# Kernel tuning notes

Hardware: AMD Instinct MI355X
Metric: run time of the kernel (lower is better)

The kernel has to match this reference:

```python
import math
import jax, jax.numpy as jnp
import numpy as np

N_NODES = 50000
N_EDGES = 600000
D = 128          # in_dim == out_dim
T = 4            # num_types
R = 4            # num_relations
H = 8            # n_heads
DK = D // H
MAX_LEN = 240    # RelTemporalEncoding max_len
EPS = 1e-5


def _sinusoid_table(n_hid, max_len):
    pos = jnp.arange(max_len, dtype=jnp.float32)[:, None]
    div = jnp.exp(jnp.arange(0, n_hid, 2, dtype=jnp.float32) * (-math.log(10000.0) / n_hid))
    s = jnp.sin(pos * div) / math.sqrt(n_hid)
    c = jnp.cos(pos * div) / math.sqrt(n_hid)
    emb = jnp.zeros((max_len, n_hid), dtype=jnp.float32)
    emb = emb.at[:, 0::2].set(s).at[:, 1::2].set(c)
    return emb


def setup_inputs() -> dict:
    key = jax.random.key(0)
    ks = jax.random.split(key, 24)
    f32 = jnp.float32
    inp = {
        'node_inp': jax.random.normal(ks[0], (N_NODES, D), dtype=f32),
        'node_type': jax.random.randint(ks[1], (N_NODES,), 0, T),
        'edge_index': jax.random.randint(ks[2], (2, N_EDGES), 0, N_NODES),
        'edge_type': jax.random.randint(ks[3], (N_EDGES,), 0, R),
        'edge_time': jax.random.randint(ks[4], (N_EDGES,), 0, MAX_LEN),
        # per-type Linear weights stored as [T, in, out] (x @ W + b)
        'Wk': jax.random.normal(ks[5], (T, D, D), dtype=f32) * 0.05,
        'bk': jnp.zeros((T, D), dtype=f32),
        'Wq': jax.random.normal(ks[6], (T, D, D), dtype=f32) * 0.05,
        'bq': jnp.zeros((T, D), dtype=f32),
        'Wv': jax.random.normal(ks[7], (T, D, D), dtype=f32) * 0.05,
        'bv': jnp.zeros((T, D), dtype=f32),
        'Wa': jax.random.normal(ks[8], (T, D, D), dtype=f32) * 0.05,
        'ba': jnp.zeros((T, D), dtype=f32),
        'gamma': jnp.ones((T, D), dtype=f32),
        'beta': jnp.zeros((T, D), dtype=f32),
        'rel_pri': jnp.ones((R, H), dtype=f32),
        'rel_att': jax.random.normal(ks[9], (R, H, DK, DK), dtype=f32) * 0.1,
        'rel_msg': jax.random.normal(ks[10], (R, H, DK, DK), dtype=f32) * 0.1,
        'skip': jnp.ones((T,), dtype=f32),
        'rte_W': jax.random.normal(ks[11], (D, D), dtype=f32) * 0.05,
        'rte_b': jnp.zeros((D,), dtype=f32),
    }
    return inp


def _type_proj(x, W, b, types):
    # all-type projection [T, N, D] then gather per-node type (T is small)
    allp = jnp.einsum('ni,tio->tno', x, W) + b[:, None, :]
    return allp[types, jnp.arange(x.shape[0])]


def reference(node_inp, node_type, edge_index, edge_type, edge_time,
              Wk, bk, Wq, bq, Wv, bv, Wa, ba, gamma, beta,
              rel_pri, rel_att, rel_msg, skip, rte_W, rte_b):
    N = node_inp.shape[0]
    E = edge_index.shape[1]
    src, tgt = edge_index[0], edge_index[1]  # j (source) -> i (target)

    # --- RelTemporalEncoding: x + Linear(emb[t]); emb is a fixed sinusoid table
    rte_out = _sinusoid_table(D, MAX_LEN) @ rte_W + rte_b  # [240, D]

    # --- per-node type-specific K/Q/V (linearity: K_t(x + rte) = K_t(x) + rte @ Wk_t)
    k_node = _type_proj(node_inp, Wk, bk, node_type)  # [N, D]
    v_node = _type_proj(node_inp, Wv, bv, node_type)
    q_node = _type_proj(node_inp, Wq, bq, node_type)
    k_rte = jnp.einsum('mi,tio->tmo', rte_out, Wk)  # [T, 240, D] (no bias; already in k_node)
    v_rte = jnp.einsum('mi,tio->tmo', rte_out, Wv)

    stype = node_type[src]
    k_e = (k_node[src] + k_rte[stype, edge_time]).reshape(E, H, DK)
    v_e = (v_node[src] + v_rte[stype, edge_time]).reshape(E, H, DK)
    q_e = q_node[tgt].reshape(E, H, DK)

    # --- per-relation head-wise transforms (R is small, fixed loop)
    k2 = jnp.zeros_like(k_e)
    msg = jnp.zeros_like(v_e)
    for r in range(R):
        sel = (edge_type == r)[:, None, None]
        k2 = jnp.where(sel, jnp.einsum('ehk,hkd->ehd', k_e, rel_att[r]), k2)
        msg = jnp.where(sel, jnp.einsum('ehk,hkd->ehd', v_e, rel_msg[r]), msg)

    logits = (q_e * k2).sum(-1) * rel_pri[edge_type] / math.sqrt(DK)  # [E, H]

    # --- softmax over edges grouped by target node
    m = jax.ops.segment_max(logits, tgt, num_segments=N)
    ex = jnp.exp(logits - m[tgt])
    den = jax.ops.segment_sum(ex, tgt, num_segments=N)
    att = ex / den[tgt]  # [E, H]

    res = (msg * att[..., None]).reshape(E, D)
    aggr = jax.ops.segment_sum(res, tgt, num_segments=N)  # [N, D]

    # --- update: per-type FFN + gated skip + per-type LayerNorm
    a = jax.nn.gelu(aggr, approximate=False)
    trans = _type_proj(a, Wa, ba, node_type)  # dropout p used in eval mode -> identity
    alpha = jax.nn.sigmoid(skip)[node_type][:, None]
    h = trans * alpha + node_inp * (1.0 - alpha)
    mu = h.mean(-1, keepdims=True)
    var = ((h - mu) ** 2).mean(-1, keepdims=True)
    out = (h - mu) / jnp.sqrt(var + EPS) * gamma[node_type] + beta[node_type]
    return out
```

## Files before the change

kernel.cpp:

```cpp
#include <hip/hip_runtime.h>
#include <hip/hip_fp16.h>
#include <math.h>

#define NH 8
#define NT 4
#define NR 4
#define MAXLEN 240

typedef __attribute__((ext_vector_type(8))) short bf16x8;
typedef __attribute__((ext_vector_type(4))) float f32x4;
typedef __attribute__((ext_vector_type(2))) float f32x2;

#if defined(__has_builtin)
#if __has_builtin(__builtin_amdgcn_cvt_pk_f32_fp8) && __has_builtin(__builtin_amdgcn_cvt_pk_fp8_f32)
#define HAS_HW_FP8 1
#endif
#endif

__device__ __forceinline__ unsigned short f2bf(float x) {
    unsigned u = __float_as_uint(x);
    u += 0x7fffu + ((u >> 16) & 1u);
    return (unsigned short)(u >> 16);
}
__device__ __forceinline__ float bflo(unsigned u) { return __uint_as_float(u << 16); }
__device__ __forceinline__ float bfhi(unsigned u) { return __uint_as_float(u & 0xffff0000u); }
__device__ __forceinline__ unsigned pack2(float a, float b) {
    return (unsigned)f2bf(a) | ((unsigned)f2bf(b) << 16);
}

__device__ __forceinline__ void fp8x4_dec(unsigned w, float* f) {
#ifdef HAS_HW_FP8
    f32x2 lo = __builtin_amdgcn_cvt_pk_f32_fp8(w, false);
    f32x2 hi = __builtin_amdgcn_cvt_pk_f32_fp8(w, true);
    f[0] = lo[0]; f[1] = lo[1]; f[2] = hi[0]; f[3] = hi[1];
#else
    unsigned ev = w & 0x00ff00ffu;
    unsigned od = (w >> 8) & 0x00ff00ffu;
    unsigned he = (((ev << 8) & 0x80008000u) | ((ev << 7) & 0x3f803f80u)) + 0x04000400u;
    unsigned ho = (((od << 8) & 0x80008000u) | ((od << 7) & 0x3f803f80u)) + 0x04000400u;
    __half2 h2e = *reinterpret_cast<__half2*>(&he);
    __half2 h2o = *reinterpret_cast<__half2*>(&ho);
    float2 fe = __half22float2(h2e);
    float2 fo = __half22float2(h2o);
    f[0] = fe.x; f[1] = fo.x; f[2] = fe.y; f[3] = fo.y;
#endif
}
__device__ __forceinline__ unsigned fp8x2_enc(float a, float b) {
#ifdef HAS_HW_FP8
    return (unsigned)__builtin_amdgcn_cvt_pk_fp8_f32(a, b, 0, false) & 0xffffu;
#else
    auto enc1 = [](float x) -> unsigned {
        float cl = fminf(fmaxf(x, -448.f), 448.f);
        __half h = __float2half(cl * 0.00390625f);
        unsigned short hr = *reinterpret_cast<unsigned short*>(&h);
        unsigned short rnd = (unsigned short)((hr & 0x7fff) + 0x3f + ((hr >> 7) & 1));
        return (unsigned)(((rnd >> 7) & 0x7f) | ((hr >> 8) & 0x80));
    };
    return enc1(a) | (enc1(b) << 8);
#endif
}

__global__ void zero_kernel(int* deg, int* cursor, int* dcnt, int* dcur, int N) {
    int i = blockIdx.x * blockDim.x + threadIdx.x;
    int stride = gridDim.x * blockDim.x;
    if (i < 256) { dcnt[i] = 0; dcur[i] = 0; }
    for (int j = i; j < N; j += stride) { deg[j] = 0; cursor[j] = 0; }
}

__global__ void deg_kernel(const int* __restrict__ ei, int* __restrict__ deg, int E) {
    int i = blockIdx.x * blockDim.x + threadIdx.x;
    int stride = gridDim.x * blockDim.x;
    for (int e = i; e < E; e += stride) atomicAdd(&deg[ei[E + e]], 1);
}

__global__ __launch_bounds__(256) void histA(const int* __restrict__ ntype,
                                             const int* __restrict__ deg,
                                             int* __restrict__ dcnt, int N) {
    __shared__ int h[256];
    int tid = threadIdx.x;
    h[tid] = 0;
    __syncthreads();
    int i = blockIdx.x * 256 + tid;
    if (i < N) atomicAdd(&h[ntype[i] * 64 + 63 - min(deg[i], 63)], 1);
    __syncthreads();
    if (h[tid]) atomicAdd(&dcnt[tid], h[tid]);
}

__global__ __launch_bounds__(256) void histB(const int* __restrict__ dcnt,
                                             int* __restrict__ dbase) {
    __shared__ int tmp[256];
    int v = dcnt[threadIdx.x];
    tmp[threadIdx.x] = v;
    __syncthreads();
    #pragma unroll
    for (int off = 1; off < 256; off <<= 1) {
        int t = threadIdx.x >= off ? tmp[threadIdx.x - off] : 0;
        __syncthreads();
        tmp[threadIdx.x] += t;
        __syncthreads();
    }
    dbase[threadIdx.x] = tmp[threadIdx.x] - v;
}

__global__ __launch_bounds__(256) void histC(const int* __restrict__ ntype,
                                             const int* __restrict__ deg,
                                             const int* __restrict__ dbase, int* __restrict__ dcur,
                                             int* __restrict__ nlist, int* __restrict__ spos,
                                             int* __restrict__ stype_s, int* __restrict__ deg_s,
                                             int N) {
    __shared__ int h[256];
    __shared__ int bb[256];
    __shared__ int cur[256];
    int tid = threadIdx.x;
    h[tid] = 0; cur[tid] = 0;
    __syncthreads();
    int i = blockIdx.x * 256 + tid;
    int b = -1, t = 0, dg = 0;
    if (i < N) {
        t = ntype[i]; dg = deg[i];
        b = t * 64 + 63 - min(dg, 63);
        atomicAdd(&h[b], 1);
    }
    __syncthreads();
    if (h[tid]) bb[tid] = atomicAdd(&dcur[tid], h[tid]);
    __syncthreads();
    if (i < N) {
        int r = atomicAdd(&cur[b], 1);
        int p = dbase[b] + bb[b] + r;
        nlist[p] = i;
        spos[i] = p;
        stype_s[p] = t;
        deg_s[p] = dg;
    }
}

__global__ __launch_bounds__(256) void scanA(const int* __restrict__ deg, int* __restrict__ excl,
                                             int* __restrict__ bsum, int N) {
    __shared__ int tmp[256];
    int i = blockIdx.x * 256 + threadIdx.x;
    int v = i < N ? deg[i] : 0;
    tmp[threadIdx.x] = v;
    __syncthreads();
    #pragma unroll
    for (int off = 1; off < 256; off <<= 1) {
        int t = threadIdx.x >= off ? tmp[threadIdx.x - off] : 0;
        __syncthreads();
        tmp[threadIdx.x] += t;
        __syncthreads();
    }
    if (i < N) excl[i] = tmp[threadIdx.x] - v;
    if (threadIdx.x == 255) bsum[blockIdx.x] = tmp[255];
}

__global__ __launch_bounds__(256) void scanB(int* __restrict__ bsum, int nb) {
    __shared__ int tmp[256];
    int v = threadIdx.x < nb ? bsum[threadIdx.x] : 0;
    tmp[threadIdx.x] = v;
    __syncthreads();
    #pragma unroll
    for (int off = 1; off < 256; off <<= 1) {
        int t = threadIdx.x >= off ? tmp[threadIdx.x - off] : 0;
        __syncthreads();
        tmp[threadIdx.x] += t;
        __syncthreads();
    }
    if (threadIdx.x < nb) bsum[threadIdx.x] = tmp[threadIdx.x] - v;
}

__global__ void scanC(const int* __restrict__ excl, const int* __restrict__ bsum,
                      int* __restrict__ row_start, int N) {
    int i = blockIdx.x * blockDim.x + threadIdx.x;
    if (i < N) row_start[i] = excl[i] + bsum[i >> 8];
}

__global__ void scatter_kernel(const int* __restrict__ ei, const int* __restrict__ etype,
                               const int* __restrict__ etime, const int* __restrict__ spos,
                               const int* __restrict__ dbase,
                               const int* __restrict__ row_start, int* __restrict__ cursor,
                               unsigned* __restrict__ ebuf, int E) {
    int tb1 = dbase[64], tb2 = dbase[128], tb3 = dbase[192];
    int i = blockIdx.x * blockDim.x + threadIdx.x;
    int stride = gridDim.x * blockDim.x;
    for (int e = i; e < E; e += stride) {
        int sps = spos[ei[e]];
        int spt = spos[ei[E + e]];
        int st = (sps >= tb1) + (sps >= tb2) + (sps >= tb3);
        int pos = atomicAdd(&cursor[spt], 1);
        ebuf[row_start[spt] + pos] =
            (unsigned)sps | ((unsigned)etype[e] << 17) | ((unsigned)etime[e] << 19) | ((unsigned)st << 27);
    }
}

__global__ __launch_bounds__(128) void rte_tables(
    const float* __restrict__ rte_W, const float* __restrict__ rte_b,
    const float* __restrict__ Wk, const float* __restrict__ Wv,
    const float* __restrict__ rel_msg,
    unsigned short* __restrict__ krte_bf, unsigned short* __restrict__ vmrte_bf) {
    int m = blockIdx.x, t = blockIdx.y, d = threadIdx.x;
    __shared__ float emb[128];
    __shared__ float sr[128];
    __shared__ float vr[128];
    int j2 = d & ~1;
    float div = expf((float)j2 * (-9.210340371976184f / 128.f));
    float ang = (float)m * div;
    emb[d] = ((d & 1) ? cosf(ang) : sinf(ang)) * 0.08838834764831845f;
    __syncthreads();
    float ro = rte_b[d];
    #pragma unroll 8
    for (int i = 0; i < 128; ++i) ro += emb[i] * rte_W[i * 128 + d];
    sr[d] = ro;
    __syncthreads();
    float ak = 0.f, av = 0.f;
    for (int i = 0; i < 128; ++i) {
        float rv = sr[i];
        ak += rv * Wk[(t * 128 + i) * 128 + d];
        av += rv * Wv[(t * 128 + i) * 128 + d];
    }
    krte_bf[(size_t)(t * MAXLEN + m) * 128 + d] = f2bf(ak);
    vr[d] = av;
    __syncthreads();
    int h = d >> 4, dd = d & 15;
    for (int r = 0; r < NR; ++r) {
        float acc = 0.f;
        #pragma unroll
        for (int k = 0; k < 16; ++k)
            acc += vr[h * 16 + k] * rel_msg[((r * NH + h) * 16 + k) * 16 + dd];
        vmrte_bf[(size_t)((t * 4 + r) * MAXLEN + m) * 128 + d] = f2bf(acc);
    }
}

__global__ __launch_bounds__(256) void pack_w9(
    const float* __restrict__ Wk, const float* __restrict__ Wq,
    const float* __restrict__ Wv, const float* __restrict__ Wa,
    const float* __restrict__ bk, const float* __restrict__ bq,
    const float* __restrict__ bv, const float* __restrict__ ba,
    const float* __restrict__ rel_att, const float* __restrict__ rel_msg,
    const float* __restrict__ rel_pri,
    short* __restrict__ PW2, float* __restrict__ PB) {
    if (blockIdx.x >= 320) {
        int bidx = (blockIdx.x - 320) * 256 + threadIdx.x;
        int col = bidx & 127, t = (bidx >> 7) & 3, set = bidx >> 9;
        int h = col >> 4, kk = col & 15;
        float val;
        if (set == 0) val = bk[t * 128 + col];
        else if (set == 9) val = ba[t * 128 + col];
        else if (set <= 4) {
            int r = set - 1;
            float pri = rel_pri[r * NH + h] * 0.25f;
            float acc = 0.f;
            #pragma unroll
            for (int dp = 0; dp < 16; ++dp)
                acc += bq[t * 128 + h * 16 + dp] * rel_att[((r * NH + h) * 16 + kk) * 16 + dp];
            val = acc * pri;
        } else {
            int r = set - 5;
            float acc = 0.f;
            #pragma unroll
            for (int kp = 0; kp < 16; ++kp)
                acc += bv[t * 128 + h * 16 + kp] * rel_msg[((r * NH + h) * 16 + kp) * 16 + kk];
            val = acc;
        }
        PB[bidx] = val;
        return;
    }
    int idx = blockIdx.x * 256 + threadIdx.x;
    int lane = idx & 63;
    int ks = (idx >> 6) & 3;
    int ctg = (idx >> 8) & 7;
    int t = (idx >> 11) & 3;
    int set = idx >> 13;
    int col = ctg * 16 + (lane & 15);
    int k0 = ks * 32 + (lane >> 4) * 8;
    int h = col >> 4, kk = col & 15;
    unsigned short o[8];
    if (set == 0 || set == 9) {
        const float* W = (set == 0 ? Wk : Wa) + t * 16384;
        #pragma unroll
        for (int j = 0; j < 8; ++j) o[j] = f2bf(W[(k0 + j) * 128 + col]);
    } else if (set <= 4) {
        int r = set - 1;
        float pri = rel_pri[r * NH + h] * 0.25f;
        float Ar[16];
        #pragma unroll
        for (int dp = 0; dp < 16; ++dp)
            Ar[dp] = rel_att[((r * NH + h) * 16 + kk) * 16 + dp] * pri;
        #pragma unroll
        for (int j = 0; j < 8; ++j) {
            const float* wr = Wq + (size_t)(t * 128 + k0 + j) * 128 + h * 16;
            float acc = 0.f;
            #pragma unroll
            for (int dp = 0; dp < 16; ++dp) acc += wr[dp] * Ar[dp];
            o[j] = f2bf(acc);
        }
    } else {
        int r = set - 5;
        float Mc[16];
        #pragma unroll
        for (int kp = 0; kp < 16; ++kp)
            Mc[kp] = rel_msg[((r * NH + h) * 16 + kp) * 16 + kk];
        #pragma unroll
        for (int j = 0; j < 8; ++j) {
            const float* wr = Wv + (size_t)(t * 128 + k0 + j) * 128 + h * 16;
            float acc = 0.f;
            #pragma unroll
            for (int kp = 0; kp < 16; ++kp) acc += wr[kp] * Mc[kp];
            o[j] = f2bf(acc);
        }
    }
    uint4 pk;
    pk.x = (unsigned)o[0] | ((unsigned)o[1] << 16);
    pk.y = (unsigned)o[2] | ((unsigned)o[3] << 16);
    pk.z = (unsigned)o[4] | ((unsigned)o[5] << 16);
    pk.w = (unsigned)o[6] | ((unsigned)o[7] << 16);
    *reinterpret_cast<uint4*>(PW2 + (size_t)idx * 8) = pk;
}

#define S8 144
#define S16 136

__global__ __launch_bounds__(256, 4) void kqv2(
    const float* __restrict__ x, const int* __restrict__ nlist_,
    const int* __restrict__ stype_s, const short* __restrict__ PW2,
    const float* __restrict__ PB,
    unsigned char* __restrict__ kn8, unsigned short* __restrict__ qa_s,
    unsigned char* __restrict__ vm8, int N) {
    __shared__ short af_l[2][4][64][8];
    __shared__ unsigned char ob8[32 * 272];
    __shared__ int st_l[32];
    unsigned short* ob16 = reinterpret_cast<unsigned short*>(ob8);
    const int tid = threadIdx.x;
    const int sp0 = blockIdx.x * 32;
    if (tid < 32) {
        int sp = sp0 + tid;
        st_l[tid] = stype_s[sp < N ? sp : N - 1];
    }
    {
        int i = tid >> 3;
        int d0 = (tid & 7) * 16;
        int sp = sp0 + i;
        int nid = nlist_[sp < N ? sp : N - 1];
        const float* xr = x + (size_t)nid * 128 + d0;
        float4 f0 = *reinterpret_cast<const float4*>(xr);
        float4 f1 = *reinterpret_cast<const float4*>(xr + 4);
        float4 f2 = *reinterpret_cast<const float4*>(xr + 8);
        float4 f3 = *reinterpret_cast<const float4*>(xr + 12);
        int m = i >> 4, rr = i & 15;
        int ks = d0 >> 5;
        int sub = (d0 >> 3) & 3;
        uint4 p0, p1;
        p0.x = pack2(f0.x, f0.y); p0.y = pack2(f0.z, f0.w);
        p0.z = pack2(f1.x, f1.y); p0.w = pack2(f1.z, f1.w);
        p1.x = pack2(f2.x, f2.y); p1.y = pack2(f2.z, f2.w);
        p1.z = pack2(f3.x, f3.y); p1.w = pack2(f3.z, f3.w);
        *reinterpret_cast<uint4*>(&af_l[m][ks][sub * 16 + rr][0]) = p0;
        *reinterpret_cast<uint4*>(&af_l[m][ks][(sub + 1) * 16 + rr][0]) = p1;
    }
    __syncthreads();

    const int lane = tid & 63, w = tid >> 6;
    const int col_l = lane & 15, rowg = lane >> 4;
    const int t0 = st_l[0], t1 = st_l[31];

    bf16x8 afr[2][4];
    #pragma unroll
    for (int m = 0; m < 2; ++m)
        #pragma unroll
        for (int ks = 0; ks < 4; ++ks)
            afr[m][ks] = *reinterpret_cast<const bf16x8*>(&af_l[m][ks][lane][0]);

    for (int set = 0; set < 9; ++set) {
        bool isf8 = (set == 0 || set >= 5);
        for (int t = t0; t <= t1; ++t) {
            #pragma unroll
            for (int c = 0; c < 2; ++c) {
                int ctg = w + c * 4;
                bf16x8 pf[4];
                #pragma unroll
                for (int ks = 0; ks < 4; ++ks)
                    pf[ks] = *reinterpret_cast<const bf16x8*>(
                        PW2 + ((size_t)((((set * 4 + t) * 8 + ctg) * 4 + ks) * 64 + lane)) * 8);
                float bval = PB[(set * 4 + t) * 128 + ctg * 16 + col_l];
                #pragma unroll
                for (int m = 0; m < 2; ++m) {
                    f32x4 acc = {0.f, 0.f, 0.f, 0.f};
                    #pragma unroll
                    for (int ks = 0; ks < 4; ++ks)
                        acc = __builtin_amdgcn_mfma_f32_16x16x32_bf16(afr[m][ks], pf[ks], acc, 0, 0, 0);
                    if (isf8) {
                        float c0 = fminf(fmaxf(acc[0] + bval, -440.f), 440.f);
                        float c1 = fminf(fmaxf(acc[1] + bval, -440.f), 440.f);
                        float c2 = fminf(fmaxf(acc[2] + bval, -440.f), 440.f);
                        float c3 = fminf(fmaxf(acc[3] + bval, -440.f), 440.f);
                        unsigned pA = fp8x2_enc(c0, c1);
                        unsigned pB = fp8x2_enc(c2, c3);
                        unsigned char by[4];
                        by[0] = (unsigned char)(pA & 0xff);
                        by[1] = (unsigned char)((pA >> 8) & 0xff);
                        by[2] = (unsigned char)(pB & 0xff);
                        by[3] = (unsigned char)((pB >> 8) & 0xff);
                        #pragma unroll
                        for (int j = 0; j < 4; ++j) {
                            int i = m * 16 + rowg * 4 + j;
                            if (st_l[i] == t)
                                ob8[i * S8 + ctg * 16 + col_l] = by[j];
                        }
                    } else {
                        #pragma unroll
                        for (int j = 0; j < 4; ++j) {
                            int i = m * 16 + rowg * 4 + j;
                            if (st_l[i] == t)
                                ob16[i * S16 + ctg * 16 + col_l] = f2bf(acc[j] + bval);
                        }
                    }
                }
            }
        }
        __syncthreads();
        if (isf8) {
            int i = tid >> 3, seg = tid & 7;
            int sp = sp0 + i;
            if (sp < N) {
                unsigned char* dst = (set == 0) ? (kn8 + (size_t)sp * 128)
                                                : (vm8 + ((size_t)sp * 4 + (set - 5)) * 128);
                *reinterpret_cast<uint4*>(dst + seg * 16) =
                    *reinterpret_cast<const uint4*>(&ob8[i * S8 + seg * 16]);
            }
        } else {
            int i = tid >> 3, d0 = (tid & 7) * 16;
            int sp = sp0 + i;
            if (sp < N) {
                unsigned short* dst = qa_s + ((size_t)sp * 4 + (set - 1)) * 128;
                const unsigned short* src = ob16 + i * S16 + d0;
                *reinterpret_cast<uint4*>(dst + d0) = *reinterpret_cast<const uint4*>(src);
                *reinterpret_cast<uint4*>(dst + d0 + 8) = *reinterpret_cast<const uint4*>(src + 8);
            }
        }
        __syncthreads();
    }
}

__global__ __launch_bounds__(256) void fused_edge_attn(
    const unsigned* __restrict__ ebuf, const int* __restrict__ row_start,
    const int* __restrict__ deg_s,
    const unsigned char* __restrict__ kn8, const unsigned short* __restrict__ krte_bf,
    const unsigned short* __restrict__ qa_s, const unsigned char* __restrict__ vm8,
    const unsigned short* __restrict__ vmrte_bf,
    unsigned short* __restrict__ aggr_bf, int N) {
    int sp = blockIdx.x * 16 + (threadIdx.x >> 4);
    int l16 = threadIdx.x & 15;
    if (sp >= N) return;
    uint4 q[4];
    #pragma unroll
    for (int r = 0; r < 4; ++r)
        q[r] = *reinterpret_cast<const uint4*>(qa_s + ((size_t)sp * 4 + r) * 128 + l16 * 8);
    int start = row_start[sp], cnt = deg_s[sp];
    float den = 0.f;
    float acc[8] = {0.f, 0.f, 0.f, 0.f, 0.f, 0.f, 0.f, 0.f};
    int i = 0;
    for (; i + 2 <= cnt; i += 2) {
        unsigned e0 = ebuf[start + i];
        unsigned e1 = ebuf[start + i + 1];
        int sps0 = e0 & 0x1ffff, r0 = (e0 >> 17) & 3, tm0 = (e0 >> 19) & 255, st0 = (e0 >> 27) & 3;
        int sps1 = e1 & 0x1ffff, r1 = (e1 >> 17) & 3, tm1 = (e1 >> 19) & 255, st1 = (e1 >> 27) & 3;
        uint2 kv0 = *reinterpret_cast<const uint2*>(kn8 + (size_t)sps0 * 128 + l16 * 8);
        uint4 kr0 = *reinterpret_cast<const uint4*>(krte_bf + (size_t)(st0 * MAXLEN + tm0) * 128 + l16 * 8);
        uint2 mv0 = *reinterpret_cast<const uint2*>(vm8 + ((size_t)sps0 * 4 + r0) * 128 + l16 * 8);
        uint4 mr0 = *reinterpret_cast<const uint4*>(vmrte_bf + (size_t)((st0 * 4 + r0) * MAXLEN + tm0) * 128 + l16 * 8);
        uint2 kv1 = *reinterpret_cast<const uint2*>(kn8 + (size_t)sps1 * 128 + l16 * 8);
        uint4 kr1 = *reinterpret_cast<const uint4*>(krte_bf + (size_t)(st1 * MAXLEN + tm1) * 128 + l16 * 8);
        uint2 mv1 = *reinterpret_cast<const uint2*>(vm8 + ((size_t)sps1 * 4 + r1) * 128 + l16 * 8);
        uint4 mr1 = *reinterpret_cast<const uint4*>(vmrte_bf + (size_t)((st1 * 4 + r1) * MAXLEN + tm1) * 128 + l16 * 8);
        float kf0[8], mf0[8], kf1[8], mf1[8];
        fp8x4_dec(kv0.x, kf0); fp8x4_dec(kv0.y, kf0 + 4);
        fp8x4_dec(mv0.x, mf0); fp8x4_dec(mv0.y, mf0 + 4);
        fp8x4_dec(kv1.x, kf1); fp8x4_dec(kv1.y, kf1 + 4);
        fp8x4_dec(mv1.x, mf1); fp8x4_dec(mv1.y, mf1 + 4);
        uint4 q0 = q[r0], q1 = q[r1];
        float p0 = (kf0[0] + bflo(kr0.x)) * bflo(q0.x) + (kf0[1] + bfhi(kr0.x)) * bfhi(q0.x)
                 + (kf0[2] + bflo(kr0.y)) * bflo(q0.y) + (kf0[3] + bfhi(kr0.y)) * bfhi(q0.y)
                 + (kf0[4] + bflo(kr0.z)) * bflo(q0.z) + (kf0[5] + bfhi(kr0.z)) * bfhi(q0.z)
                 + (kf0[6] + bflo(kr0.w)) * bflo(q0.w) + (kf0[7] + bfhi(kr0.w)) * bfhi(q0.w);
        float p1 = (kf1[0] + bflo(kr1.x)) * bflo(q1.x) + (kf1[1] + bfhi(kr1.x)) * bfhi(q1.x)
                 + (kf1[2] + bflo(kr1.y)) * bflo(q1.y) + (kf1[3] + bfhi(kr1.y)) * bfhi(q1.y)
                 + (kf1[4] + bflo(kr1.z)) * bflo(q1.z) + (kf1[5] + bfhi(kr1.z)) * bfhi(q1.z)
                 + (kf1[6] + bflo(kr1.w)) * bflo(q1.w) + (kf1[7] + bfhi(kr1.w)) * bfhi(q1.w);
        p0 += __shfl_xor(p0, 1);
        p1 += __shfl_xor(p1, 1);
        float w0 = __expf(p0), w1 = __expf(p1);
        den += w0 + w1;
        acc[0] += w0 * (mf0[0] + bflo(mr0.x)) + w1 * (mf1[0] + bflo(mr1.x));
        acc[1] += w0 * (mf0[1] + bfhi(mr0.x)) + w1 * (mf1[1] + bfhi(mr1.x));
        acc[2] += w0 * (mf0[2] + bflo(mr0.y)) + w1 * (mf1[2] + bflo(mr1.y));
        acc[3] += w0 * (mf0[3] + bfhi(mr0.y)) + w1 * (mf1[3] + bfhi(mr1.y));
        acc[4] += w0 * (mf0[4] + bflo(mr0.z)) + w1 * (mf1[4] + bflo(mr1.z));
        acc[5] += w0 * (mf0[5] + bfhi(mr0.z)) + w1 * (mf1[5] + bfhi(mr1.z));
        acc[6] += w0 * (mf0[6] + bflo(mr0.w)) + w1 * (mf1[6] + bflo(mr1.w));
        acc[7] += w0 * (mf0[7] + bfhi(mr0.w)) + w1 * (mf1[7] + bfhi(mr1.w));
    }
    if (i < cnt) {
        unsigned e0 = ebuf[start + i];
        int sps0 = e0 & 0x1ffff, r0 = (e0 >> 17) & 3, tm0 = (e0 >> 19) & 255, st0 = (e0 >> 27) & 3;
        uint2 kv0 = *reinterpret_cast<const uint2*>(kn8 + (size_t)sps0 * 128 + l16 * 8);
        uint4 kr0 = *reinterpret_cast<const uint4*>(krte_bf + (size_t)(st0 * MAXLEN + tm0) * 128 + l16 * 8);
        uint2 mv0 = *reinterpret_cast<const uint2*>(vm8 + ((size_t)sps0 * 4 + r0) * 128 + l16 * 8);
        uint4 mr0 = *reinterpret_cast<const uint4*>(vmrte_bf + (size_t)((st0 * 4 + r0) * MAXLEN + tm0) * 128 + l16 * 8);
        float kf0[8], mf0[8];
        fp8x4_dec(kv0.x, kf0); fp8x4_dec(kv0.y, kf0 + 4);
        fp8x4_dec(mv0.x, mf0); fp8x4_dec(mv0.y, mf0 + 4);
        uint4 q0 = q[r0];
        float p0 = (kf0[0] + bflo(kr0.x)) * bflo(q0.x) + (kf0[1] + bfhi(kr0.x)) * bfhi(q0.x)
                 + (kf0[2] + bflo(kr0.y)) * bflo(q0.y) + (kf0[3] + bfhi(kr0.y)) * bfhi(q0.y)
                 + (kf0[4] + bflo(kr0.z)) * bflo(q0.z) + (kf0[5] + bfhi(kr0.z)) * bfhi(q0.z)
                 + (kf0[6] + bflo(kr0.w)) * bflo(q0.w) + (kf0[7] + bfhi(kr0.w)) * bfhi(q0.w);
        p0 += __shfl_xor(p0, 1);
        float w0 = __expf(p0);
        den += w0;
        acc[0] += w0 * (mf0[0] + bflo(mr0.x));
        acc[1] += w0 * (mf0[1] + bfhi(mr0.x));
        acc[2] += w0 * (mf0[2] + bflo(mr0.y));
        acc[3] += w0 * (mf0[3] + bfhi(mr0.y));
        acc[4] += w0 * (mf0[4] + bflo(mr0.z));
        acc[5] += w0 * (mf0[5] + bfhi(mr0.z));
        acc[6] += w0 * (mf0[6] + bflo(mr0.w));
        acc[7] += w0 * (mf0[7] + bfhi(mr0.w));
    }
    float inv = den > 0.f ? 1.f / den : 0.f;
    uint4 o;
    o.x = pack2(acc[0] * inv, acc[1] * inv);
    o.y = pack2(acc[2] * inv, acc[3] * inv);
    o.z = pack2(acc[4] * inv, acc[5] * inv);
    o.w = pack2(acc[6] * inv, acc[7] * inv);
    *reinterpret_cast<uint4*>(aggr_bf + (size_t)sp * 128 + l16 * 8) = o;
}

__global__ __launch_bounds__(256, 4) void update_sorted(
    const float* __restrict__ x, const int* __restrict__ nlist_,
    const int* __restrict__ stype_s, const short* __restrict__ PW2,
    const float* __restrict__ PB, const float* __restrict__ gamma,
    const float* __restrict__ beta, const float* __restrict__ skip,
    const unsigned short* __restrict__ aggr_bf, float* __restrict__ out, int N) {
    __shared__ short af_l[2][4][64][8];
    __shared__ float hs[32][128];
    __shared__ int st_l[32];
    __shared__ int nid_l[32];
    const int tid = threadIdx.x;
    const int sp0 = blockIdx.x * 32;
    if (tid < 32) {
        int sp = sp0 + tid;
        int spc = sp < N ? sp : N - 1;
        st_l[tid] = stype_s[spc];
        nid_l[tid] = nlist_[spc];
    }
    {
        int i = tid >> 3;
        int d0 = (tid & 7) * 16;
        int spc = sp0 + i < N ? sp0 + i : N - 1;
        const unsigned short* ar = aggr_bf + (size_t)spc * 128 + d0;
        uint4 v0 = *reinterpret_cast<const uint4*>(ar);
        uint4 v1 = *reinterpret_cast<const uint4*>(ar + 8);
        unsigned vv[8] = {v0.x, v0.y, v0.z, v0.w, v1.x, v1.y, v1.z, v1.w};
        float g[16];
        #pragma unroll
        for (int c = 0; c < 8; ++c) {
            float a0 = bflo(vv[c]), a1 = bfhi(vv[c]);
            g[c * 2 + 0] = 0.5f * a0 * (1.f + erff(a0 * 0.7071067811865476f));
            g[c * 2 + 1] = 0.5f * a1 * (1.f + erff(a1 * 0.7071067811865476f));
        }
        int m = i >> 4, rr = i & 15;
        int ks = d0 >> 5;
        int sub = (d0 >> 3) & 3;
        uint4 p0, p1;
        p0.x = pack2(g[0], g[1]);  p0.y = pack2(g[2], g[3]);
        p0.z = pack2(g[4], g[5]);  p0.w = pack2(g[6], g[7]);
        p1.x = pack2(g[8], g[9]);  p1.y = pack2(g[10], g[11]);
        p1.z = pack2(g[12], g[13]); p1.w = pack2(g[14], g[15]);
        *reinterpret_cast<uint4*>(&af_l[m][ks][sub * 16 + rr][0]) = p0;
        *reinterpret_cast<uint4*>(&af_l[m][ks][(sub + 1) * 16 + rr][0]) = p1;
    }
    __syncthreads();

    const int lane = tid & 63, w = tid >> 6;
    const int col_l = lane & 15, rowg = lane >> 4;
    const int t0 = st_l[0], t1 = st_l[31];

    bf16x8 afr[2][4];
    #pragma unroll
    for (int m = 0; m < 2; ++m)
        #pragma unroll
        for (int ks = 0; ks < 4; ++ks)
            afr[m][ks] = *reinterpret_cast<const bf16x8*>(&af_l[m][ks][lane][0]);

    for (int t = t0; t <= t1; ++t) {
        #pragma unroll
        for (int c = 0; c < 2; ++c) {
            int ctg = w + c * 4;
            bf16x8 pf[4];
            #pragma unroll
            for (int ks = 0; ks < 4; ++ks)
                pf[ks] = *reinterpret_cast<const bf16x8*>(
                    PW2 + ((size_t)((((9 * 4 + t) * 8 + ctg) * 4 + ks) * 64 + lane)) * 8);
            float bval = PB[(9 * 4 + t) * 128 + ctg * 16 + col_l];
            #pragma unroll
            for (int m = 0; m < 2; ++m) {
                f32x4 acc = {0.f, 0.f, 0.f, 0.f};
                #pragma unroll
                for (int ks = 0; ks < 4; ++ks)
                    acc = __builtin_amdgcn_mfma_f32_16x16x32_bf16(afr[m][ks], pf[ks], acc, 0, 0, 0);
                #pragma unroll
                for (int j = 0; j < 4; ++j) {
                    int i = m * 16 + rowg * 4 + j;
                    if (st_l[i] == t)
                        hs[i][ctg * 16 + col_l] = acc[j] + bval;
                }
            }
        }
    }
    __syncthreads();

    {
        int i = tid >> 3;
        int d0 = (tid & 7) * 16;
        int sp = sp0 + i;
        int nid = nid_l[i];
        int t = st_l[i];
        float alpha = 1.f / (1.f + expf(-skip[t]));
        const float* xr = x + (size_t)nid * 128 + d0;
        float hv[16];
        float s1 = 0.f, s2 = 0.f;
        #pragma unroll
        for (int c = 0; c < 4; ++c) {
            float4 xf = *reinterpret_cast<const float4*>(xr + c * 4);
            float4 tf;
            tf.x = hs[i][d0 + c * 4 + 0]; tf.y = hs[i][d0 + c * 4 + 1];
            tf.z = hs[i][d0 + c * 4 + 2]; tf.w = hs[i][d0 + c * 4 + 3];
            hv[c * 4 + 0] = tf.x * alpha + xf.x * (1.f - alpha);
            hv[c * 4 + 1] = tf.y * alpha + xf.y * (1.f - alpha);
            hv[c * 4 + 2] = tf.z * alpha + xf.z * (1.f - alpha);
            hv[c * 4 + 3] = tf.w * alpha + xf.w * (1.f - alpha);
            #pragma unroll
            for (int j = 0; j < 4; ++j) { s1 += hv[c * 4 + j]; s2 += hv[c * 4 + j] * hv[c * 4 + j]; }
        }
        #pragma unroll
        for (int off = 1; off < 8; off <<= 1) {
            s1 += __shfl_xor(s1, off);
            s2 += __shfl_xor(s2, off);
        }
        float mu = s1 * (1.f / 128.f);
        float var = s2 * (1.f / 128.f) - mu * mu;
        float inv = 1.f / sqrtf(var + 1e-5f);
        if (sp < N) {
            float* orow = out + (size_t)nid * 128 + d0;
            const float* gr = gamma + t * 128 + d0;
            const float* br = beta + t * 128 + d0;
            #pragma unroll
            for (int c = 0; c < 4; ++c) {
                float4 gf = *reinterpret_cast<const float4*>(gr + c * 4);
                float4 bf = *reinterpret_cast<const float4*>(br + c * 4);
                float4 of;
                of.x = (hv[c * 4 + 0] - mu) * inv * gf.x + bf.x;
                of.y = (hv[c * 4 + 1] - mu) * inv * gf.y + bf.y;
                of.z = (hv[c * 4 + 2] - mu) * inv * gf.z + bf.z;
                of.w = (hv[c * 4 + 3] - mu) * inv * gf.w + bf.w;
                *reinterpret_cast<float4*>(orow + c * 4) = of;
            }
        }
    }
}

extern "C" void kernel_launch(void* const* d_in, const int* in_sizes, int n_in,
                              void* d_out, int out_size, void* d_ws, size_t ws_size,
                              hipStream_t stream) {
    const float* node_inp = (const float*)d_in[0];
    const int*   node_type = (const int*)d_in[1];
    const int*   edge_index = (const int*)d_in[2];
    const int*   edge_type = (const int*)d_in[3];
    const int*   edge_time = (const int*)d_in[4];
    const float* Wk = (const float*)d_in[5];
    const float* bk = (const float*)d_in[6];
    const float* Wq = (const float*)d_in[7];
    const float* bq = (const float*)d_in[8];
    const float* Wv = (const float*)d_in[9];
    const float* bv = (const float*)d_in[10];
    const float* Wa = (const float*)d_in[11];
    const float* ba = (const float*)d_in[12];
    const float* gamma = (const float*)d_in[13];
    const float* beta = (const float*)d_in[14];
    const float* rel_pri = (const float*)d_in[15];
    const float* rel_att = (const float*)d_in[16];
    const float* rel_msg = (const float*)d_in[17];
    const float* skip = (const float*)d_in[18];
    const float* rte_W = (const float*)d_in[19];
    const float* rte_b = (const float*)d_in[20];

    int N = in_sizes[0] / 128;
    int E = in_sizes[3];

    char* base = (char*)d_ws;
    unsigned short* aggr_bf = (unsigned short*)base;  base += (size_t)N * 128 * 2;
    unsigned char* kn8 = (unsigned char*)base;        base += (size_t)N * 128;
    unsigned char* vm8 = (unsigned char*)base;        base += (size_t)N * 4 * 128;
    unsigned short* qa_s = (unsigned short*)base;     base += (size_t)N * 4 * 128 * 2;
    unsigned short* krte_bf = (unsigned short*)base;  base += (size_t)NT * MAXLEN * 128 * 2;
    unsigned short* vmrte_bf = (unsigned short*)base; base += (size_t)NT * NR * MAXLEN * 128 * 2;
    short* PW2 = (short*)base;                base += (size_t)10 * NT * 128 * 128 * 2;
    float* PB = (float*)base;                 base += (size_t)10 * NT * 128 * 4;
    int* deg = (int*)base;                    base += (size_t)N * 4;
    int* deg_s = (int*)base;                  base += (size_t)N * 4;
    int* cursor = (int*)base;                 base += (size_t)N * 4;
    int* excl = (int*)base;                   base += (size_t)N * 4;
    int* row_start = (int*)base;              base += (size_t)N * 4;
    int* nlist = (int*)base;                  base += (size_t)N * 4;
    int* spos = (int*)base;                   base += (size_t)N * 4;
    int* stype_s = (int*)base;                base += (size_t)N * 4;
    int* bsum = (int*)base;                   base += 256 * 4;
    int* dcnt = (int*)base;                   base += 256 * 4;
    int* dcur = (int*)base;                   base += 256 * 4;
    int* dbase = (int*)base;                  base += 256 * 4;
    base = (char*)(((size_t)base + 15) & ~(size_t)15);
    unsigned* ebuf = (unsigned*)base;         base += (size_t)E * 4;

    int nb = (N + 255) / 256;
    int ng = (N + 255) / 256;

    zero_kernel<<<256, 256, 0, stream>>>(deg, cursor, dcnt, dcur, N);
    deg_kernel<<<1024, 256, 0, stream>>>(edge_index, deg, E);
    histA<<<ng, 256, 0, stream>>>(node_type, deg, dcnt, N);
    histB<<<1, 256, 0, stream>>>(dcnt, dbase);
    histC<<<ng, 256, 0, stream>>>(node_type, deg, dbase, dcur, nlist, spos, stype_s, deg_s, N);
    scanA<<<nb, 256, 0, stream>>>(deg_s, excl, bsum, N);
    scanB<<<1, 256, 0, stream>>>(bsum, nb);
    scanC<<<nb, 256, 0, stream>>>(excl, bsum, row_start, N);
    scatter_kernel<<<1024, 256, 0, stream>>>(edge_index, edge_type, edge_time, spos, dbase,
                                             row_start, cursor, ebuf, E);
    dim3 gt(MAXLEN, NT);
    rte_tables<<<gt, 128, 0, stream>>>(rte_W, rte_b, Wk, Wv, rel_msg, krte_bf, vmrte_bf);
    pack_w9<<<340, 256, 0, stream>>>(Wk, Wq, Wv, Wa, bk, bq, bv, ba,
                                     rel_att, rel_msg, rel_pri, PW2, PB);
    kqv2<<<(N + 31) / 32, 256, 0, stream>>>(node_inp, nlist, stype_s, PW2, PB,
                                            kn8, qa_s, vm8, N);
    fused_edge_attn<<<(N + 15) / 16, 256, 0, stream>>>(ebuf, row_start, deg_s,
                                                       kn8, krte_bf, qa_s, vm8, vmrte_bf,
                                                       aggr_bf, N);
    update_sorted<<<(N + 31) / 32, 256, 0, stream>>>(node_inp, nlist, stype_s, PW2, PB,
                                                     gamma, beta, skip, aggr_bf, (float*)d_out, N);
}
```

Baseline: 234.5 us.

## Interleave fp8 K and VM per relation; store RTE tables as fp8

```diff
diff --git a/kernel.cpp b/kernel.cpp
--- a/kernel.cpp
+++ b/kernel.cpp
@@ -195,7 +195,7 @@
     const float* __restrict__ rte_W, const float* __restrict__ rte_b,
     const float* __restrict__ Wk, const float* __restrict__ Wv,
     const float* __restrict__ rel_msg,
-    unsigned short* __restrict__ krte_bf, unsigned short* __restrict__ vmrte_bf) {
+    unsigned char* __restrict__ rtec8) {
     int m = blockIdx.x, t = blockIdx.y, d = threadIdx.x;
     __shared__ float emb[128];
     __shared__ float sr[128];
@@ -216,16 +216,22 @@
         ak += rv * Wk[(t * 128 + i) * 128 + d];
         av += rv * Wv[(t * 128 + i) * 128 + d];
     }
-    krte_bf[(size_t)(t * MAXLEN + m) * 128 + d] = f2bf(ak);
+    unsigned char kb = (unsigned char)(fp8x2_enc(fminf(fmaxf(ak, -440.f), 440.f), 0.f) & 0xff);
+    int koff = (d >> 3) * 16 + 8 + (d & 7);
+    #pragma unroll
+    for (int r = 0; r < NR; ++r)
+        rtec8[(size_t)((t * 4 + r) * MAXLEN + m) * 256 + koff] = kb;
     vr[d] = av;
     __syncthreads();
     int h = d >> 4, dd = d & 15;
+    int voff = (d >> 3) * 16 + (d & 7);
     for (int r = 0; r < NR; ++r) {
         float acc = 0.f;
         #pragma unroll
         for (int k = 0; k < 16; ++k)
             acc += vr[h * 16 + k] * rel_msg[((r * NH + h) * 16 + k) * 16 + dd];
-        vmrte_bf[(size_t)((t * 4 + r) * MAXLEN + m) * 128 + d] = f2bf(acc);
+        unsigned char vb = (unsigned char)(fp8x2_enc(fminf(fmaxf(acc, -440.f), 440.f), 0.f) & 0xff);
+        rtec8[(size_t)((t * 4 + r) * MAXLEN + m) * 256 + voff] = vb;
     }
 }
 
@@ -317,15 +323,16 @@
 
 #define S8 144
 #define S16 136
+#define KST 144
 
 __global__ __launch_bounds__(256, 4) void kqv2(
     const float* __restrict__ x, const int* __restrict__ nlist_,
     const int* __restrict__ stype_s, const short* __restrict__ PW2,
     const float* __restrict__ PB,
-    unsigned char* __restrict__ kn8, unsigned short* __restrict__ qa_s,
-    unsigned char* __restrict__ vm8, int N) {
+    unsigned char* __restrict__ knvm8, unsigned short* __restrict__ qa_s, int N) {
     __shared__ short af_l[2][4][64][8];
     __shared__ unsigned char ob8[32 * 272];
+    __shared__ unsigned char kn_keep[32 * KST];
     __shared__ int st_l[32];
     unsigned short* ob16 = reinterpret_cast<unsigned short*>(ob8);
     const int tid = threadIdx.x;
@@ -416,14 +423,25 @@
             }
         }
         __syncthreads();
-        if (isf8) {
+        if (set == 0) {
+            int i = tid >> 3, seg = tid & 7;
+            *reinterpret_cast<uint4*>(&kn_keep[i * KST + seg * 16]) =
+                *reinterpret_cast<const uint4*>(&ob8[i * S8 + seg * 16]);
+        } else if (set >= 5) {
             int i = tid >> 3, seg = tid & 7;
             int sp = sp0 + i;
             if (sp < N) {
-                unsigned char* dst = (set == 0) ? (kn8 + (size_t)sp * 128)
-                                                : (vm8 + ((size_t)sp * 4 + (set - 5)) * 128);
-                *reinterpret_cast<uint4*>(dst + seg * 16) =
-                    *reinterpret_cast<const uint4*>(&ob8[i * S8 + seg * 16]);
+                int r = set - 5;
+                unsigned char* dst = knvm8 + (size_t)(sp * 4 + r) * 256;
+                #pragma unroll
+                for (int cc = 0; cc < 2; ++cc) {
+                    int c = seg * 2 + cc;
+                    uint2 vmc = *reinterpret_cast<const uint2*>(&ob8[i * S8 + c * 8]);
+                    uint2 knc = *reinterpret_cast<const uint2*>(&kn_keep[i * KST + c * 8]);
+                    uint4 outv;
+                    outv.x = vmc.x; outv.y = vmc.y; outv.z = knc.x; outv.w = knc.y;
+                    *reinterpret_cast<uint4*>(dst + c * 16) = outv;
+                }
             }
         } else {
             int i = tid >> 3, d0 = (tid & 7) * 16;
@@ -442,9 +460,8 @@
 __global__ __launch_bounds__(256) void fused_edge_attn(
     const unsigned* __restrict__ ebuf, const int* __restrict__ row_start,
     const int* __restrict__ deg_s,
-    const unsigned char* __restrict__ kn8, const unsigned short* __restrict__ krte_bf,
-    const unsigned short* __restrict__ qa_s, const unsigned char* __restrict__ vm8,
-    const unsigned short* __restrict__ vmrte_bf,
+    const unsigned char* __restrict__ knvm8, const unsigned char* __restrict__ rtec8,
+    const unsigned short* __restrict__ qa_s,
     unsigned short* __restrict__ aggr_bf, int N) {
     int sp = blockIdx.x * 16 + (threadIdx.x >> 4);
     int l16 = threadIdx.x & 15;
@@ -462,67 +479,58 @@
         unsigned e1 = ebuf[start + i + 1];
         int sps0 = e0 & 0x1ffff, r0 = (e0 >> 17) & 3, tm0 = (e0 >> 19) & 255, st0 = (e0 >> 27) & 3;
         int sps1 = e1 & 0x1ffff, r1 = (e1 >> 17) & 3, tm1 = (e1 >> 19) & 255, st1 = (e1 >> 27) & 3;
-        uint2 kv0 = *reinterpret_cast<const uint2*>(kn8 + (size_t)sps0 * 128 + l16 * 8);
-        uint4 kr0 = *reinterpret_cast<const uint4*>(krte_bf + (size_t)(st0 * MAXLEN + tm0) * 128 + l16 * 8);
-        uint2 mv0 = *reinterpret_cast<const uint2*>(vm8 + ((size_t)sps0 * 4 + r0) * 128 + l16 * 8);
-        uint4 mr0 = *reinterpret_cast<const uint4*>(vmrte_bf + (size_t)((st0 * 4 + r0) * MAXLEN + tm0) * 128 + l16 * 8);
-        uint2 kv1 = *reinterpret_cast<const uint2*>(kn8 + (size_t)sps1 * 128 + l16 * 8);
-        uint4 kr1 = *reinterpret_cast<const uint4*>(krte_bf + (size_t)(st1 * MAXLEN + tm1) * 128 + l16 * 8);
-        uint2 mv1 = *reinterpret_cast<const uint2*>(vm8 + ((size_t)sps1 * 4 + r1) * 128 + l16 * 8);
-        uint4 mr1 = *reinterpret_cast<const uint4*>(vmrte_bf + (size_t)((st1 * 4 + r1) * MAXLEN + tm1) * 128 + l16 * 8);
-        float kf0[8], mf0[8], kf1[8], mf1[8];
-        fp8x4_dec(kv0.x, kf0); fp8x4_dec(kv0.y, kf0 + 4);
-        fp8x4_dec(mv0.x, mf0); fp8x4_dec(mv0.y, mf0 + 4);
-        fp8x4_dec(kv1.x, kf1); fp8x4_dec(kv1.y, kf1 + 4);
-        fp8x4_dec(mv1.x, mf1); fp8x4_dec(mv1.y, mf1 + 4);
+        uint4 g10 = *reinterpret_cast<const uint4*>(knvm8 + (size_t)(sps0 * 4 + r0) * 256 + l16 * 16);
+        uint4 g20 = *reinterpret_cast<const uint4*>(rtec8 + (size_t)((st0 * 4 + r0) * MAXLEN + tm0) * 256 + l16 * 16);
+        uint4 g11 = *reinterpret_cast<const uint4*>(knvm8 + (size_t)(sps1 * 4 + r1) * 256 + l16 * 16);
+        uint4 g21 = *reinterpret_cast<const uint4*>(rtec8 + (size_t)((st1 * 4 + r1) * MAXLEN + tm1) * 256 + l16 * 16);
+        float mf0[8], kf0[8], mr0[8], kr0[8];
+        float mf1[8], kf1[8], mr1[8], kr1[8];
+        fp8x4_dec(g10.x, mf0); fp8x4_dec(g10.y, mf0 + 4);
+        fp8x4_dec(g10.z, kf0); fp8x4_dec(g10.w, kf0 + 4);
+        fp8x4_dec(g20.x, mr0); fp8x4_dec(g20.y, mr0 + 4);
+        fp8x4_dec(g20.z, kr0); fp8x4_dec(g20.w, kr0 + 4);
+        fp8x4_dec(g11.x, mf1); fp8x4_dec(g11.y, mf1 + 4);
+        fp8x4_dec(g11.z, kf1); fp8x4_dec(g11.w, kf1 + 4);
+        fp8x4_dec(g21.x, mr1); fp8x4_dec(g21.y, mr1 + 4);
+        fp8x4_dec(g21.z, kr1); fp8x4_dec(g21.w, kr1 + 4);
         uint4 q0 = q[r0], q1 = q[r1];
-        float p0 = (kf0[0] + bflo(kr0.x)) * bflo(q0.x) + (kf0[1] + bfhi(kr0.x)) * bfhi(q0.x)
-                 + (kf0[2] + bflo(kr0.y)) * bflo(q0.y) + (kf0[3] + bfhi(kr0.y)) * bfhi(q0.y)
-                 + (kf0[4] + bflo(kr0.z)) * bflo(q0.z) + (kf0[5] + bfhi(kr0.z)) * bfhi(q0.z)
-                 + (kf0[6] + bflo(kr0.w)) * bflo(q0.w) + (kf0[7] + bfhi(kr0.w)) * bfhi(q0.w);
-        float p1 = (kf1[0] + bflo(kr1.x)) * bflo(q1.x) + (kf1[1] + bfhi(kr1.x)) * bfhi(q1.x)
-                 + (kf1[2] + bflo(kr1.y)) * bflo(q1.y) + (kf1[3] + bfhi(kr1.y)) * bfhi(q1.y)
-                 + (kf1[4] + bflo(kr1.z)) * bflo(q1.z) + (kf1[5] + bfhi(kr1.z)) * bfhi(q1.z)
-                 + (kf1[6] + bflo(kr1.w)) * bflo(q1.w) + (kf1[7] + bfhi(kr1.w)) * bfhi(q1.w);
+        float p0 = (kf0[0] + kr0[0]) * bflo(q0.x) + (kf0[1] + kr0[1]) * bfhi(q0.x)
+                 + (kf0[2] + kr0[2]) * bflo(q0.y) + (kf0[3] + kr0[3]) * bfhi(q0.y)
+                 + (kf0[4] + kr0[4]) * bflo(q0.z) + (kf0[5] + kr0[5]) * bfhi(q0.z)
+                 + (kf0[6] + kr0[6]) * bflo(q0.w) + (kf0[7] + kr0[7]) * bfhi(q0.w);
+        float p1 = (kf1[0] + kr1[0]) * bflo(q1.x) + (kf1[1] + kr1[1]) * bfhi(q1.x)
+                 + (kf1[2] + kr1[2]) * bflo(q1.y) + (kf1[3] + kr1[3]) * bfhi(q1.y)
+                 + (kf1[4] + kr1[4]) * bflo(q1.z) + (kf1[5] + kr1[5]) * bfhi(q1.z)
+                 + (kf1[6] + kr1[6]) * bflo(q1.w) + (kf1[7] + kr1[7]) * bfhi(q1.w);
         p0 += __shfl_xor(p0, 1);
         p1 += __shfl_xor(p1, 1);
         float w0 = __expf(p0), w1 = __expf(p1);
         den += w0 + w1;
-        acc[0] += w0 * (mf0[0] + bflo(mr0.x)) + w1 * (mf1[0] + bflo(mr1.x));
-        acc[1] += w0 * (mf0[1] + bfhi(mr0.x)) + w1 * (mf1[1] + bfhi(mr1.x));
-        acc[2] += w0 * (mf0[2] + bflo(mr0.y)) + w1 * (mf1[2] + bflo(mr1.y));
-        acc[3] += w0 * (mf0[3] + bfhi(mr0.y)) + w1 * (mf1[3] + bfhi(mr1.y));
-        acc[4] += w0 * (mf0[4] + bflo(mr0.z)) + w1 * (mf1[4] + bflo(mr1.z));
-        acc[5] += w0 * (mf0[5] + bfhi(mr0.z)) + w1 * (mf1[5] + bfhi(mr1.z));
-        acc[6] += w0 * (mf0[6] + bflo(mr0.w)) + w1 * (mf1[6] + bflo(mr1.w));
-        acc[7] += w0 * (mf0[7] + bfhi(mr0.w)) + w1 * (mf1[7] + bfhi(mr1.w));
+        #pragma unroll
+        for (int j = 0; j < 8; ++j)
+            acc[j] += w0 * (mf0[j] + mr0[j]) + w1 * (mf1[j] + mr1[j]);
     }
     if (i < cnt) {
         unsigned e0 = ebuf[start + i];
         int sps0 = e0 & 0x1ffff, r0 = (e0 >> 17) & 3, tm0 = (e0 >> 19) & 255, st0 = (e0 >> 27) & 3;
-        uint2 kv0 = *reinterpret_cast<const uint2*>(kn8 + (size_t)sps0 * 128 + l16 * 8);
-        uint4 kr0 = *reinterpret_cast<const uint4*>(krte_bf + (size_t)(st0 * MAXLEN + tm0) * 128 + l16 * 8);
-        uint2 mv0 = *reinterpret_cast<const uint2*>(vm8 + ((size_t)sps0 * 4 + r0) * 128 + l16 * 8);
-        uint4 mr0 = *reinterpret_cast<const uint4*>(vmrte_bf + (size_t)((st0 * 4 + r0) * MAXLEN + tm0) * 128 + l16 * 8);
-        float kf0[8], mf0[8];
-        fp8x4_dec(kv0.x, kf0); fp8x4_dec(kv0.y, kf0 + 4);
-        fp8x4_dec(mv0.x, mf0); fp8x4_dec(mv0.y, mf0 + 4);
+        uint4 g10 = *reinterpret_cast<const uint4*>(knvm8 + (size_t)(sps0 * 4 + r0) * 256 + l16 * 16);
+        uint4 g20 = *reinterpret_cast<const uint4*>(rtec8 + (size_t)((st0 * 4 + r0) * MAXLEN + tm0) * 256 + l16 * 16);
+        float mf0[8], kf0[8], mr0[8], kr0[8];
+        fp8x4_dec(g10.x, mf0); fp8x4_dec(g10.y, mf0 + 4);
+        fp8x4_dec(g10.z, kf0); fp8x4_dec(g10.w, kf0 + 4);
+        fp8x4_dec(g20.x, mr0); fp8x4_dec(g20.y, mr0 + 4);
+        fp8x4_dec(g20.z, kr0); fp8x4_dec(g20.w, kr0 + 4);
         uint4 q0 = q[r0];
-        float p0 = (kf0[0] + bflo(kr0.x)) * bflo(q0.x) + (kf0[1] + bfhi(kr0.x)) * bfhi(q0.x)
-                 + (kf0[2] + bflo(kr0.y)) * bflo(q0.y) + (kf0[3] + bfhi(kr0.y)) * bfhi(q0.y)
-                 + (kf0[4] + bflo(kr0.z)) * bflo(q0.z) + (kf0[5] + bfhi(kr0.z)) * bfhi(q0.z)
-                 + (kf0[6] + bflo(kr0.w)) * bflo(q0.w) + (kf0[7] + bfhi(kr0.w)) * bfhi(q0.w);
+        float p0 = (kf0[0] + kr0[0]) * bflo(q0.x) + (kf0[1] + kr0[1]) * bfhi(q0.x)
+                 + (kf0[2] + kr0[2]) * bflo(q0.y) + (kf0[3] + kr0[3]) * bfhi(q0.y)
+                 + (kf0[4] + kr0[4]) * bflo(q0.z) + (kf0[5] + kr0[5]) * bfhi(q0.z)
+                 + (kf0[6] + kr0[6]) * bflo(q0.w) + (kf0[7] + kr0[7]) * bfhi(q0.w);
         p0 += __shfl_xor(p0, 1);
         float w0 = __expf(p0);
         den += w0;
-        acc[0] += w0 * (mf0[0] + bflo(mr0.x));
-        acc[1] += w0 * (mf0[1] + bfhi(mr0.x));
-        acc[2] += w0 * (mf0[2] + bflo(mr0.y));
-        acc[3] += w0 * (mf0[3] + bfhi(mr0.y));
-        acc[4] += w0 * (mf0[4] + bflo(mr0.z));
-        acc[5] += w0 * (mf0[5] + bfhi(mr0.z));
-        acc[6] += w0 * (mf0[6] + bflo(mr0.w));
-        acc[7] += w0 * (mf0[7] + bfhi(mr0.w));
+        #pragma unroll
+        for (int j = 0; j < 8; ++j)
+            acc[j] += w0 * (mf0[j] + mr0[j]);
     }
     float inv = den > 0.f ? 1.f / den : 0.f;
     uint4 o;
@@ -696,12 +704,10 @@
     int E = in_sizes[3];
 
     char* base = (char*)d_ws;
+    unsigned char* knvm8 = (unsigned char*)base;      base += (size_t)N * 4 * 256;
+    unsigned short* qa_s = (unsigned short*)base;     base += (size_t)N * 4 * 128 * 2;
     unsigned short* aggr_bf = (unsigned short*)base;  base += (size_t)N * 128 * 2;
-    unsigned char* kn8 = (unsigned char*)base;        base += (size_t)N * 128;
-    unsigned char* vm8 = (unsigned char*)base;        base += (size_t)N * 4 * 128;
-    unsigned short* qa_s = (unsigned short*)base;     base += (size_t)N * 4 * 128 * 2;
-    unsigned short* krte_bf = (unsigned short*)base;  base += (size_t)NT * MAXLEN * 128 * 2;
-    unsigned short* vmrte_bf = (unsigned short*)base; base += (size_t)NT * NR * MAXLEN * 128 * 2;
+    unsigned char* rtec8 = (unsigned char*)base;      base += (size_t)NT * NR * MAXLEN * 256;
     short* PW2 = (short*)base;                base += (size_t)10 * NT * 128 * 128 * 2;
     float* PB = (float*)base;                 base += (size_t)10 * NT * 128 * 4;
     int* deg = (int*)base;                    base += (size_t)N * 4;
@@ -733,14 +739,13 @@
     scatter_kernel<<<1024, 256, 0, stream>>>(edge_index, edge_type, edge_time, spos, dbase,
                                              row_start, cursor, ebuf, E);
     dim3 gt(MAXLEN, NT);
-    rte_tables<<<gt, 128, 0, stream>>>(rte_W, rte_b, Wk, Wv, rel_msg, krte_bf, vmrte_bf);
+    rte_tables<<<gt, 128, 0, stream>>>(rte_W, rte_b, Wk, Wv, rel_msg, rtec8);
     pack_w9<<<340, 256, 0, stream>>>(Wk, Wq, Wv, Wa, bk, bq, bv, ba,
                                      rel_att, rel_msg, rel_pri, PW2, PB);
     kqv2<<<(N + 31) / 32, 256, 0, stream>>>(node_inp, nlist, stype_s, PW2, PB,
-                                            kn8, qa_s, vm8, N);
+                                            knvm8, qa_s, N);
     fused_edge_attn<<<(N + 15) / 16, 256, 0, stream>>>(ebuf, row_start, deg_s,
-                                                       kn8, krte_bf, qa_s, vm8, vmrte_bf,
-                                                       aggr_bf, N);
+                                                       knvm8, rtec8, qa_s, aggr_bf, N);
     update_sorted<<<(N + 31) / 32, 256, 0, stream>>>(node_inp, nlist, stype_s, PW2, PB,
                                                      gamma, beta, skip, aggr_bf, (float*)d_out, N);
 }
```

Result: no change. 238.7 us (+1.8%).
